# Kernel optimization log

Measured on AMD Instinct MI355X. Metric: run time of the kernel, lower is better.

Reference implementation:

```python
import jax, jax.numpy as jnp
import numpy as np

N_NODES = 20000
N_EDGES = 640000
D = 128


def setup_inputs() -> dict:
    key = jax.random.key(0)
    ks = jax.random.split(key, 8)
    scale = 1.0 / np.sqrt(D)
    x = jax.random.normal(ks[0], (N_NODES, D), dtype=jnp.float32)
    edge_index = jax.random.randint(ks[1], (2, N_EDGES), 0, N_NODES, dtype=jnp.int64)
    W1_rel = jax.random.normal(ks[2], (D, D), dtype=jnp.float32) * scale
    b1_rel = jnp.zeros((D,), dtype=jnp.float32)
    W1_root = jax.random.normal(ks[3], (D, D), dtype=jnp.float32) * scale
    W2_rel = jax.random.normal(ks[4], (D, D), dtype=jnp.float32) * scale
    b2_rel = jnp.zeros((D,), dtype=jnp.float32)
    W2_root = jax.random.normal(ks[5], (D, D), dtype=jnp.float32) * scale
    return {"x": x, "edge_index": edge_index,
            "W1_rel": W1_rel, "b1_rel": b1_rel, "W1_root": W1_root,
            "W2_rel": W2_rel, "b2_rel": b2_rel, "W2_root": W2_root}


def _graph_conv(x, src, dst, W_rel, b_rel, W_root):
    # sum-aggregate neighbor features: gather from src, scatter-add to dst
    agg = jax.ops.segment_sum(x[src], dst, num_segments=N_NODES)  # [N, D]
    # PyG GraphConv: lin_rel(agg) (with bias) + lin_root(x) (no bias)
    return agg @ W_rel + b_rel + x @ W_root


def reference(x, edge_index, W1_rel, b1_rel, W1_root, W2_rel, b2_rel, W2_root):
    src, dst = edge_index[0], edge_index[1]  # messages flow src (j) -> dst (i)
    h = jax.nn.relu(_graph_conv(x, src, dst, W1_rel, b1_rel, W1_root))
    out = _graph_conv(h, src, dst, W2_rel, b2_rel, W2_root)  # final ReLU stripped
    return out
```

## Files before the change

kernel.cpp:

```cpp
#include <hip/hip_runtime.h>

#define N_NODES 20000
#define N_EDGES 640000
#define D 128
#define CAP 128
#define NBINS 157
#define PA_BLOCKS 256
#define EPB 2500
#define SLABCAP 40

typedef __attribute__((ext_vector_type(8))) short bf16x8;
typedef __attribute__((ext_vector_type(4))) float f32x4;

__device__ __forceinline__ short f2bf(float f) {
    union { float f; unsigned u; } un; un.f = f;
    unsigned r = un.u + 0x7fff + ((un.u >> 16) & 1);
    return (short)(r >> 16);
}
__device__ __forceinline__ float bflo(unsigned u) { return __uint_as_float(u << 16); }
__device__ __forceinline__ float bfhi(unsigned u) { return __uint_as_float(u & 0xffff0000u); }

__global__ __launch_bounds__(256) void prep_kernel(
    const float* __restrict__ x,
    const int* __restrict__ src, const int* __restrict__ dst,
    const float* __restrict__ W1_rel, const float* __restrict__ W1_root,
    const float* __restrict__ W2_rel, const float* __restrict__ W2_root,
    unsigned* __restrict__ binned, int* __restrict__ cnts,
    short* __restrict__ xb, short* __restrict__ wpk1, short* __restrict__ wpk2)
{
    const int b = blockIdx.x;
    const int tid = threadIdx.x;
    if (b < PA_BLOCKS) {
        __shared__ int sOff[NBINS];
        for (int i = tid; i < NBINS; i += 256) sOff[i] = 0;
        __syncthreads();
        const int e0 = b * EPB;
        for (int idx = tid; idx < EPB; idx += 256) {
            int d = dst[e0 + idx];
            int s = src[e0 + idx];
            int bin = d >> 7;
            int off = atomicAdd(&sOff[bin], 1);
            if (off < SLABCAP)
                binned[(size_t)(bin * PA_BLOCKS + b) * SLABCAP + off] =
                    ((unsigned)(d & 127) << 16) | (unsigned)s;
        }
        __syncthreads();
        for (int i = tid; i < NBINS; i += 256) {
            int c = sOff[i];
            cnts[i * PA_BLOCKS + b] = (c > SLABCAP) ? SLABCAP : c;
        }
    } else if (b < PA_BLOCKS + 2500) {
        int i = (b - PA_BLOCKS) * 256 + tid;
        float4 v = ((const float4*)x)[i];
        ushort4 o;
        o.x = (unsigned short)f2bf(v.x);
        o.y = (unsigned short)f2bf(v.y);
        o.z = (unsigned short)f2bf(v.z);
        o.w = (unsigned short)f2bf(v.w);
        ((ushort4*)xb)[i] = o;
    } else {
        int pb  = b - (PA_BLOCKS + 2500);
        int job = pb >> 4;
        int idx = (pb & 15) * 256 + tid;
        const float* Wrel  = job ? W2_rel  : W1_rel;
        const float* Wroot = job ? W2_root : W1_root;
        short* Wpk = job ? wpk2 : wpk1;
        int lane = idx & 63;
        int ct   = (idx >> 6) & 7;
        int t    = idx >> 9;
        const float* W = (t < 4) ? Wrel : Wroot;
        int k0  = (t & 3) * 32 + (lane >> 4) * 8;
        int col = ct * 16 + (lane & 15);
        bf16x8 pk;
#pragma unroll
        for (int j = 0; j < 8; j++)
            pk[j] = f2bf(W[(size_t)(k0 + j) * D + col]);
        ((bf16x8*)Wpk)[idx] = pk;
    }
}

__global__ __launch_bounds__(256) void binplace_kernel(
    const unsigned* __restrict__ binned, const int* __restrict__ cnts,
    unsigned short* __restrict__ buckets, int* __restrict__ cnt)
{
    __shared__ int lcnt[128];
    const int bin = blockIdx.x;
    const int tid = threadIdx.x;
    if (tid < 128) lcnt[tid] = 0;
    __syncthreads();
    int c = cnts[bin * PA_BLOCKS + tid];
    const unsigned* rec = binned + (size_t)(bin * PA_BLOCKS + tid) * SLABCAP;
    for (int i = 0; i < c; i++) {
        unsigned u = rec[i];
        int nl = (int)(u >> 16);
        int slot = atomicAdd(&lcnt[nl], 1);
        if (slot < CAP)
            buckets[(((bin << 7) | nl) << 7) + slot] = (unsigned short)(u & 0xffffu);
    }
    __syncthreads();
    int node = (bin << 7) + tid;
    if (tid < 128 && node < N_NODES) {
        int n = lcnt[tid];
        cnt[node] = (n > CAP) ? CAP : n;
    }
}

template <bool RELU, bool OUT_BF16>
__global__ __launch_bounds__(512) void layer_kernel(
    const short* __restrict__ xin,
    const int* __restrict__ cnt,
    const unsigned short* __restrict__ buckets,
    const short* __restrict__ Wpk,
    const float* __restrict__ brel,
    void* __restrict__ outp)
{
    __shared__ short sAgg[16][136];

    const int tid = threadIdx.x;

    for (int half = 0; half < 2; half++) {
        const int bin  = blockIdx.x * 2 + half;
        const int row0 = bin * 16;
        if (half) __syncthreads();

        {
            const int hw   = tid >> 5;
            const int lane = tid & 31;
            const int node = row0 + hw;
            int n = cnt[node];
            n = (n > CAP) ? CAP : n;
            uint2 idxpk = *(const uint2*)(buckets + (node << 7) + lane * 4);

            float4 acc = make_float4(0.f, 0.f, 0.f, 0.f);
            int full8 = n & ~7;
            int i = 0;
            for (; i < full8; i += 8) {
                int baseLane = i >> 2;
                uint2 u[8];
#pragma unroll
                for (int q = 0; q < 8; q++) {
                    unsigned word = __shfl((q & 2) ? idxpk.y : idxpk.x,
                                           baseLane + (q >> 2), 32);
                    unsigned sidx = (q & 1) ? (word >> 16) : (word & 0xffffu);
                    u[q] = *(const uint2*)(xin + (size_t)sidx * D + lane * 4);
                }
#pragma unroll
                for (int q = 0; q < 8; q++) {
                    acc.x += bflo(u[q].x); acc.y += bfhi(u[q].x);
                    acc.z += bflo(u[q].y); acc.w += bfhi(u[q].y);
                }
            }
            if (i < n) {
                uint2 u[8];
#pragma unroll
                for (int q = 0; q < 8; q++) {
                    int j  = i + q;
                    int jc = (j < n) ? j : (n - 1);
                    unsigned word = __shfl((jc & 2) ? idxpk.y : idxpk.x,
                                           jc >> 2, 32);
                    unsigned sidx = (jc & 1) ? (word >> 16) : (word & 0xffffu);
                    u[q] = *(const uint2*)(xin + (size_t)sidx * D + lane * 4);
                }
#pragma unroll
                for (int q = 0; q < 8; q++) {
                    float m = (i + q < n) ? 1.f : 0.f;
                    acc.x += m * bflo(u[q].x); acc.y += m * bfhi(u[q].x);
                    acc.z += m * bflo(u[q].y); acc.w += m * bfhi(u[q].y);
                }
            }
            ushort4 o;
            o.x = (unsigned short)f2bf(acc.x);
            o.y = (unsigned short)f2bf(acc.y);
            o.z = (unsigned short)f2bf(acc.z);
            o.w = (unsigned short)f2bf(acc.w);
            *(ushort4*)&sAgg[hw][lane * 4] = o;
        }
        __syncthreads();

        const int wave = tid >> 6;
        const int lane = tid & 63;
        const int quad = lane >> 4;
        const int l16  = lane & 15;

        f32x4 acc = (f32x4){0.f, 0.f, 0.f, 0.f};
        const short* arow_x = xin + (size_t)(row0 + l16) * D + quad * 8;
        const bf16x8* wb = (const bf16x8*)Wpk + lane;

#pragma unroll
        for (int t = 0; t < 8; t++) {
            bf16x8 a;
            if (t < 4)
                a = *(const bf16x8*)&sAgg[l16][(t & 3) * 32 + quad * 8];
            else
                a = *(const bf16x8*)(arow_x + (t & 3) * 32);
            bf16x8 bfr = wb[(t * 8 + wave) * 64];
            acc = __builtin_amdgcn_mfma_f32_16x16x32_bf16(a, bfr, acc, 0, 0, 0);
        }

        const int col  = wave * 16 + l16;
        const int orow = row0 + quad * 4;
        const float bias = brel[col];
#pragma unroll
        for (int r = 0; r < 4; r++) {
            float v = acc[r] + bias;
            if (RELU) v = fmaxf(v, 0.f);
            if (OUT_BF16)
                ((short*)outp)[(size_t)(orow + r) * D + col] = f2bf(v);
            else
                ((float*)outp)[(size_t)(orow + r) * D + col] = v;
        }
    }
}

extern "C" void kernel_launch(void* const* d_in, const int* in_sizes, int n_in,
                              void* d_out, int out_size, void* d_ws, size_t ws_size,
                              hipStream_t stream) {
    const float* x       = (const float*)d_in[0];
    const int*   ei      = (const int*)  d_in[1];
    const float* W1_rel  = (const float*)d_in[2];
    const float* b1_rel  = (const float*)d_in[3];
    const float* W1_root = (const float*)d_in[4];
    const float* W2_rel  = (const float*)d_in[5];
    const float* b2_rel  = (const float*)d_in[6];
    const float* W2_root = (const float*)d_in[7];
    float* out = (float*)d_out;

    char* p = (char*)d_ws;
    short* xb   = (short*)p;  p += (size_t)N_NODES * D * 2;
    short* hb   = (short*)p;  p += (size_t)N_NODES * D * 2;
    short* wpk1 = (short*)p;  p += 65536;
    short* wpk2 = (short*)p;  p += 65536;
    int*   cnt  = (int*)p;    p += (size_t)N_NODES * 4;
    unsigned short* buckets = (unsigned short*)p;
    p += (size_t)NBINS * 128 * CAP * 2;
    unsigned* binned = (unsigned*)p;
    p += (size_t)NBINS * PA_BLOCKS * SLABCAP * 4;
    int* cnts = (int*)p;

    const int* src = ei;
    const int* dst = ei + N_EDGES;

    prep_kernel<<<PA_BLOCKS + 2500 + 32, 256, 0, stream>>>(
        x, src, dst, W1_rel, W1_root, W2_rel, W2_root,
        binned, cnts, xb, wpk1, wpk2);

    binplace_kernel<<<NBINS, 256, 0, stream>>>(binned, cnts, buckets, cnt);

    layer_kernel<true, true><<<625, 512, 0, stream>>>(
        xb, cnt, buckets, wpk1, b1_rel, (void*)hb);

    layer_kernel<false, false><<<625, 512, 0, stream>>>(
        hb, cnt, buckets, wpk2, b2_rel, (void*)out);
}
```

Before: 151.4 us.

## Fuse all stages into one persistent kernel with software grid barriers

Replaces the four separate launches (prep, binplace, two layer kernels) with a single persistent kernel of 512 blocks. Stages are separated by a spin-wait grid barrier on global atomics, reset each call by a memset. The edge binning is repartitioned to 512 blocks with smaller slabs, and the layer loop becomes grid-strided. This removes launch gaps and inter-kernel drain, but it depends on all blocks being co-resident, serialises the binplace stage onto 157 blocks while the rest wait, and the smaller slab capacity may drop edges for heavier bins.

```diff
diff --git a/kernel.cpp b/kernel.cpp
--- a/kernel.cpp
+++ b/kernel.cpp
@@ -5,9 +5,11 @@
 #define D 128
 #define CAP 128
 #define NBINS 157
-#define PA_BLOCKS 256
-#define EPB 2500
-#define SLABCAP 40
+#define NBLK 512
+#define NTHR 512
+#define EPB 1250
+#define SLABCAP 24
+#define LBINS (N_NODES / 16)
 
 typedef __attribute__((ext_vector_type(8))) short bf16x8;
 typedef __attribute__((ext_vector_type(4))) float f32x4;
@@ -20,108 +22,41 @@
 __device__ __forceinline__ float bflo(unsigned u) { return __uint_as_float(u << 16); }
 __device__ __forceinline__ float bfhi(unsigned u) { return __uint_as_float(u & 0xffff0000u); }
 
-__global__ __launch_bounds__(256) void prep_kernel(
-    const float* __restrict__ x,
-    const int* __restrict__ src, const int* __restrict__ dst,
-    const float* __restrict__ W1_rel, const float* __restrict__ W1_root,
-    const float* __restrict__ W2_rel, const float* __restrict__ W2_root,
-    unsigned* __restrict__ binned, int* __restrict__ cnts,
-    short* __restrict__ xb, short* __restrict__ wpk1, short* __restrict__ wpk2)
-{
-    const int b = blockIdx.x;
-    const int tid = threadIdx.x;
-    if (b < PA_BLOCKS) {
-        __shared__ int sOff[NBINS];
-        for (int i = tid; i < NBINS; i += 256) sOff[i] = 0;
-        __syncthreads();
-        const int e0 = b * EPB;
-        for (int idx = tid; idx < EPB; idx += 256) {
-            int d = dst[e0 + idx];
-            int s = src[e0 + idx];
-            int bin = d >> 7;
-            int off = atomicAdd(&sOff[bin], 1);
-            if (off < SLABCAP)
-                binned[(size_t)(bin * PA_BLOCKS + b) * SLABCAP + off] =
-                    ((unsigned)(d & 127) << 16) | (unsigned)s;
-        }
-        __syncthreads();
-        for (int i = tid; i < NBINS; i += 256) {
-            int c = sOff[i];
-            cnts[i * PA_BLOCKS + b] = (c > SLABCAP) ? SLABCAP : c;
-        }
-    } else if (b < PA_BLOCKS + 2500) {
-        int i = (b - PA_BLOCKS) * 256 + tid;
-        float4 v = ((const float4*)x)[i];
-        ushort4 o;
-        o.x = (unsigned short)f2bf(v.x);
-        o.y = (unsigned short)f2bf(v.y);
-        o.z = (unsigned short)f2bf(v.z);
-        o.w = (unsigned short)f2bf(v.w);
-        ((ushort4*)xb)[i] = o;
-    } else {
-        int pb  = b - (PA_BLOCKS + 2500);
-        int job = pb >> 4;
-        int idx = (pb & 15) * 256 + tid;
-        const float* Wrel  = job ? W2_rel  : W1_rel;
-        const float* Wroot = job ? W2_root : W1_root;
-        short* Wpk = job ? wpk2 : wpk1;
-        int lane = idx & 63;
-        int ct   = (idx >> 6) & 7;
-        int t    = idx >> 9;
-        const float* W = (t < 4) ? Wrel : Wroot;
-        int k0  = (t & 3) * 32 + (lane >> 4) * 8;
-        int col = ct * 16 + (lane & 15);
-        bf16x8 pk;
-#pragma unroll
-        for (int j = 0; j < 8; j++)
-            pk[j] = f2bf(W[(size_t)(k0 + j) * D + col]);
-        ((bf16x8*)Wpk)[idx] = pk;
-    }
-}
-
-__global__ __launch_bounds__(256) void binplace_kernel(
-    const unsigned* __restrict__ binned, const int* __restrict__ cnts,
-    unsigned short* __restrict__ buckets, int* __restrict__ cnt)
-{
-    __shared__ int lcnt[128];
-    const int bin = blockIdx.x;
-    const int tid = threadIdx.x;
-    if (tid < 128) lcnt[tid] = 0;
+union ShMem {
+    int   sOff[NBINS];
+    int   lcnt[128];
+    short sAgg[16][136];
+};
+
+__device__ __forceinline__ void grid_barrier(int* bar_cnt, int* bar_gen) {
     __syncthreads();
-    int c = cnts[bin * PA_BLOCKS + tid];
-    const unsigned* rec = binned + (size_t)(bin * PA_BLOCKS + tid) * SLABCAP;
-    for (int i = 0; i < c; i++) {
-        unsigned u = rec[i];
-        int nl = (int)(u >> 16);
-        int slot = atomicAdd(&lcnt[nl], 1);
-        if (slot < CAP)
-            buckets[(((bin << 7) | nl) << 7) + slot] = (unsigned short)(u & 0xffffu);
+    if (threadIdx.x == 0) {
+        __threadfence();
+        int g = atomicAdd(bar_gen, 0);
+        if (atomicAdd(bar_cnt, 1) == NBLK - 1) {
+            atomicExch(bar_cnt, 0);
+            atomicAdd(bar_gen, 1);
+        } else {
+            while (atomicAdd(bar_gen, 0) == g)
+                __builtin_amdgcn_s_sleep(8);
+        }
+        __threadfence();
     }
     __syncthreads();
-    int node = (bin << 7) + tid;
-    if (tid < 128 && node < N_NODES) {
-        int n = lcnt[tid];
-        cnt[node] = (n > CAP) ? CAP : n;
-    }
 }
 
 template <bool RELU, bool OUT_BF16>
-__global__ __launch_bounds__(512) void layer_kernel(
-    const short* __restrict__ xin,
-    const int* __restrict__ cnt,
+__device__ __forceinline__ void do_layer(
+    short (*sAgg)[136],
+    const short* __restrict__ xin, const int* __restrict__ cnt,
     const unsigned short* __restrict__ buckets,
-    const short* __restrict__ Wpk,
-    const float* __restrict__ brel,
+    const short* __restrict__ Wpk, const float* __restrict__ brel,
     void* __restrict__ outp)
 {
-    __shared__ short sAgg[16][136];
-
     const int tid = threadIdx.x;
-
-    for (int half = 0; half < 2; half++) {
-        const int bin  = blockIdx.x * 2 + half;
+    for (int bin = blockIdx.x; bin < LBINS; bin += NBLK) {
         const int row0 = bin * 16;
-        if (half) __syncthreads();
+        if (bin != (int)blockIdx.x) __syncthreads();
 
         {
             const int hw   = tid >> 5;
@@ -210,6 +145,106 @@
                 ((float*)outp)[(size_t)(orow + r) * D + col] = v;
         }
     }
+}
+
+__global__ __launch_bounds__(NTHR, 4) void mega_kernel(
+    const float* __restrict__ x,
+    const int* __restrict__ src, const int* __restrict__ dst,
+    const float* __restrict__ W1_rel, const float* __restrict__ W1_root,
+    const float* __restrict__ W2_rel, const float* __restrict__ W2_root,
+    const float* __restrict__ b1_rel, const float* __restrict__ b2_rel,
+    unsigned* __restrict__ binned, int* __restrict__ cnts,
+    unsigned short* __restrict__ buckets, int* __restrict__ cnt,
+    short* __restrict__ xb, short* __restrict__ hb,
+    short* __restrict__ wpk1, short* __restrict__ wpk2,
+    int* __restrict__ bar_cnt, int* __restrict__ bar_gen,
+    float* __restrict__ out)
+{
+    __shared__ ShMem sh;
+    const int b   = blockIdx.x;
+    const int tid = threadIdx.x;
+
+    {
+        for (int i = tid; i < NBINS; i += NTHR) sh.sOff[i] = 0;
+        __syncthreads();
+        const int e0 = b * EPB;
+        for (int idx = tid; idx < EPB; idx += NTHR) {
+            int d = dst[e0 + idx];
+            int s = src[e0 + idx];
+            int bin = d >> 7;
+            int off = atomicAdd(&sh.sOff[bin], 1);
+            if (off < SLABCAP)
+                binned[((size_t)b * NBINS + bin) * SLABCAP + off] =
+                    ((unsigned)(d & 127) << 16) | (unsigned)s;
+        }
+        __syncthreads();
+        for (int i = tid; i < NBINS; i += NTHR) {
+            int c = sh.sOff[i];
+            cnts[b * NBINS + i] = (c > SLABCAP) ? SLABCAP : c;
+        }
+    }
+    {
+        const int gtid = b * NTHR + tid;
+        for (int i = gtid; i < N_NODES * D / 4; i += NBLK * NTHR) {
+            float4 v = ((const float4*)x)[i];
+            ushort4 o;
+            o.x = (unsigned short)f2bf(v.x);
+            o.y = (unsigned short)f2bf(v.y);
+            o.z = (unsigned short)f2bf(v.z);
+            o.w = (unsigned short)f2bf(v.w);
+            ((ushort4*)xb)[i] = o;
+        }
+    }
+    {
+        const int gtid = b * NTHR + tid;
+        if (gtid < 8192) {
+            int job = gtid >> 12;
+            int idx = gtid & 4095;
+            const float* Wrel  = job ? W2_rel  : W1_rel;
+            const float* Wroot = job ? W2_root : W1_root;
+            short* Wpk = job ? wpk2 : wpk1;
+            int lane = idx & 63;
+            int ct   = (idx >> 6) & 7;
+            int t    = idx >> 9;
+            const float* W = (t < 4) ? Wrel : Wroot;
+            int k0  = (t & 3) * 32 + (lane >> 4) * 8;
+            int col = ct * 16 + (lane & 15);
+            bf16x8 pk;
+#pragma unroll
+            for (int j = 0; j < 8; j++)
+                pk[j] = f2bf(W[(size_t)(k0 + j) * D + col]);
+            ((bf16x8*)Wpk)[idx] = pk;
+        }
+    }
+    grid_barrier(bar_cnt, bar_gen);
+
+    if (b < NBINS) {
+        if (tid < 128) sh.lcnt[tid] = 0;
+        __syncthreads();
+        const int bin = b;
+        int c = cnts[tid * NBINS + bin];
+        const unsigned* rec = binned + ((size_t)tid * NBINS + bin) * SLABCAP;
+        for (int i = 0; i < c; i++) {
+            unsigned u = rec[i];
+            int nl = (int)(u >> 16);
+            int slot = atomicAdd(&sh.lcnt[nl], 1);
+            if (slot < CAP)
+                buckets[(((bin << 7) | nl) << 7) + slot] =
+                    (unsigned short)(u & 0xffffu);
+        }
+        __syncthreads();
+        int node = (bin << 7) + tid;
+        if (tid < 128 && node < N_NODES) {
+            int n = sh.lcnt[tid];
+            cnt[node] = (n > CAP) ? CAP : n;
+        }
+    }
+    grid_barrier(bar_cnt, bar_gen);
+
+    do_layer<true, true>(sh.sAgg, xb, cnt, buckets, wpk1, b1_rel, (void*)hb);
+    grid_barrier(bar_cnt, bar_gen);
+
+    do_layer<false, false>(sh.sAgg, hb, cnt, buckets, wpk2, b2_rel, (void*)out);
 }
 
 extern "C" void kernel_launch(void* const* d_in, const int* in_sizes, int n_in,
@@ -234,21 +269,18 @@
     unsigned short* buckets = (unsigned short*)p;
     p += (size_t)NBINS * 128 * CAP * 2;
     unsigned* binned = (unsigned*)p;
-    p += (size_t)NBINS * PA_BLOCKS * SLABCAP * 4;
-    int* cnts = (int*)p;
+    p += (size_t)NBLK * NBINS * SLABCAP * 4;
+    int* cnts = (int*)p;      p += (size_t)NBLK * NBINS * 4;
+    int* bar  = (int*)p;
+    int* bar_cnt = bar;
+    int* bar_gen = bar + 32;
 
     const int* src = ei;
     const int* dst = ei + N_EDGES;
 
-    prep_kernel<<<PA_BLOCKS + 2500 + 32, 256, 0, stream>>>(
-        x, src, dst, W1_rel, W1_root, W2_rel, W2_root,
-        binned, cnts, xb, wpk1, wpk2);
-
-    binplace_kernel<<<NBINS, 256, 0, stream>>>(binned, cnts, buckets, cnt);
-
-    layer_kernel<true, true><<<625, 512, 0, stream>>>(
-        xb, cnt, buckets, wpk1, b1_rel, (void*)hb);
-
-    layer_kernel<false, false><<<625, 512, 0, stream>>>(
-        hb, cnt, buckets, wpk2, b2_rel, (void*)out);
-}
+    hipMemsetAsync(bar, 0, 256, stream);
+    mega_kernel<<<NBLK, NTHR, 0, stream>>>(
+        x, src, dst, W1_rel, W1_root, W2_rel, W2_root, b1_rel, b2_rel,
+        binned, cnts, buckets, cnt, xb, hb, wpk1, wpk2,
+        bar_cnt, bar_gen, out);
+}
```

Result: slower. 205.1 us (+35.5%).

## Split neighbor lists by source half and gather halves in phased order

Applied to the files above, without the earlier changes.

The bin placement now stores sources below 10000 from the front of each node's bucket and sources at or above 10000 from the back, packing both counts into cnt. The layer kernel gathers the low-index sources first, hits a block barrier, then gathers the high-index sources, so all waves in a block touch a narrower slice of the feature table at a time for better cache locality. The layer kernel also drops its two-bins-per-block loop and launches twice as many blocks, one 16-row bin each. The extra barrier in the middle of the gather adds synchronisation and can stall waves whose nodes have uneven low/high counts.

```diff
diff --git a/kernel.cpp b/kernel.cpp
--- a/kernel.cpp
+++ b/kernel.cpp
@@ -8,6 +8,7 @@
 #define PA_BLOCKS 256
 #define EPB 2500
 #define SLABCAP 40
+#define SRC_SPLIT 10000
 
 typedef __attribute__((ext_vector_type(8))) short bf16x8;
 typedef __attribute__((ext_vector_type(4))) float f32x4;
@@ -83,25 +84,75 @@
     const unsigned* __restrict__ binned, const int* __restrict__ cnts,
     unsigned short* __restrict__ buckets, int* __restrict__ cnt)
 {
-    __shared__ int lcnt[128];
+    __shared__ int lo[128];
+    __shared__ int hi[128];
     const int bin = blockIdx.x;
     const int tid = threadIdx.x;
-    if (tid < 128) lcnt[tid] = 0;
+    if (tid < 128) { lo[tid] = 0; hi[tid] = 0; }
     __syncthreads();
     int c = cnts[bin * PA_BLOCKS + tid];
     const unsigned* rec = binned + (size_t)(bin * PA_BLOCKS + tid) * SLABCAP;
     for (int i = 0; i < c; i++) {
         unsigned u = rec[i];
         int nl = (int)(u >> 16);
-        int slot = atomicAdd(&lcnt[nl], 1);
-        if (slot < CAP)
-            buckets[(((bin << 7) | nl) << 7) + slot] = (unsigned short)(u & 0xffffu);
+        unsigned s = u & 0xffffu;
+        if ((int)s < SRC_SPLIT) {
+            int slot = atomicAdd(&lo[nl], 1);
+            if (slot < CAP)
+                buckets[(((bin << 7) | nl) << 7) + slot] = (unsigned short)s;
+        } else {
+            int slot = CAP - 1 - atomicAdd(&hi[nl], 1);
+            if (slot >= 0)
+                buckets[(((bin << 7) | nl) << 7) + slot] = (unsigned short)s;
+        }
     }
     __syncthreads();
     int node = (bin << 7) + tid;
     if (tid < 128 && node < N_NODES) {
-        int n = lcnt[tid];
-        cnt[node] = (n > CAP) ? CAP : n;
+        int nlo = lo[tid]; if (nlo > CAP) nlo = CAP;
+        int nhi = hi[tid]; if (nhi > CAP - nlo) nhi = CAP - nlo;
+        cnt[node] = nlo | (nhi << 16);
+    }
+}
+
+__device__ __forceinline__ void gather_range(
+    float4& acc, const short* __restrict__ xin,
+    uint2 idxpk, int lane, int start, int count)
+{
+    const int end = start + count;
+    int k = start;
+    const int full_end = start + (count & ~7);
+    for (; k < full_end; k += 8) {
+        uint2 u[8];
+#pragma unroll
+        for (int q = 0; q < 8; q++) {
+            int j = k + q;
+            unsigned word = __shfl((j & 2) ? idxpk.y : idxpk.x, j >> 2, 32);
+            unsigned sidx = (j & 1) ? (word >> 16) : (word & 0xffffu);
+            u[q] = *(const uint2*)(xin + (size_t)sidx * D + lane * 4);
+        }
+#pragma unroll
+        for (int q = 0; q < 8; q++) {
+            acc.x += bflo(u[q].x); acc.y += bfhi(u[q].x);
+            acc.z += bflo(u[q].y); acc.w += bfhi(u[q].y);
+        }
+    }
+    if (k < end) {
+        uint2 u[8];
+#pragma unroll
+        for (int q = 0; q < 8; q++) {
+            int j  = k + q;
+            int jc = (j < end) ? j : (end - 1);
+            unsigned word = __shfl((jc & 2) ? idxpk.y : idxpk.x, jc >> 2, 32);
+            unsigned sidx = (jc & 1) ? (word >> 16) : (word & 0xffffu);
+            u[q] = *(const uint2*)(xin + (size_t)sidx * D + lane * 4);
+        }
+#pragma unroll
+        for (int q = 0; q < 8; q++) {
+            float m = (k + q < end) ? 1.f : 0.f;
+            acc.x += m * bflo(u[q].x); acc.y += m * bfhi(u[q].x);
+            acc.z += m * bflo(u[q].y); acc.w += m * bfhi(u[q].y);
+        }
     }
 }
 
@@ -116,99 +167,63 @@
 {
     __shared__ short sAgg[16][136];
 
-    const int tid = threadIdx.x;
-
-    for (int half = 0; half < 2; half++) {
-        const int bin  = blockIdx.x * 2 + half;
-        const int row0 = bin * 16;
-        if (half) __syncthreads();
-
-        {
-            const int hw   = tid >> 5;
-            const int lane = tid & 31;
-            const int node = row0 + hw;
-            int n = cnt[node];
-            n = (n > CAP) ? CAP : n;
-            uint2 idxpk = *(const uint2*)(buckets + (node << 7) + lane * 4);
-
-            float4 acc = make_float4(0.f, 0.f, 0.f, 0.f);
-            int full8 = n & ~7;
-            int i = 0;
-            for (; i < full8; i += 8) {
-                int baseLane = i >> 2;
-                uint2 u[8];
-#pragma unroll
-                for (int q = 0; q < 8; q++) {
-                    unsigned word = __shfl((q & 2) ? idxpk.y : idxpk.x,
-                                           baseLane + (q >> 2), 32);
-                    unsigned sidx = (q & 1) ? (word >> 16) : (word & 0xffffu);
-                    u[q] = *(const uint2*)(xin + (size_t)sidx * D + lane * 4);
-                }
-#pragma unroll
-                for (int q = 0; q < 8; q++) {
-                    acc.x += bflo(u[q].x); acc.y += bfhi(u[q].x);
-                    acc.z += bflo(u[q].y); acc.w += bfhi(u[q].y);
-                }
-            }
-            if (i < n) {
-                uint2 u[8];
-#pragma unroll
-                for (int q = 0; q < 8; q++) {
-                    int j  = i + q;
-                    int jc = (j < n) ? j : (n - 1);
-                    unsigned word = __shfl((jc & 2) ? idxpk.y : idxpk.x,
-                                           jc >> 2, 32);
-                    unsigned sidx = (jc & 1) ? (word >> 16) : (word & 0xffffu);
-                    u[q] = *(const uint2*)(xin + (size_t)sidx * D + lane * 4);
-                }
-#pragma unroll
-                for (int q = 0; q < 8; q++) {
-                    float m = (i + q < n) ? 1.f : 0.f;
-                    acc.x += m * bflo(u[q].x); acc.y += m * bfhi(u[q].x);
-                    acc.z += m * bflo(u[q].y); acc.w += m * bfhi(u[q].y);
-                }
-            }
-            ushort4 o;
-            o.x = (unsigned short)f2bf(acc.x);
-            o.y = (unsigned short)f2bf(acc.y);
-            o.z = (unsigned short)f2bf(acc.z);
-            o.w = (unsigned short)f2bf(acc.w);
-            *(ushort4*)&sAgg[hw][lane * 4] = o;
-        }
+    const int tid  = threadIdx.x;
+    const int row0 = blockIdx.x * 16;
+
+    {
+        const int hw   = tid >> 5;
+        const int lane = tid & 31;
+        const int node = row0 + hw;
+        int nc  = cnt[node];
+        int nlo = nc & 0xffff;
+        int nhi = nc >> 16;
+        uint2 idxpk = *(const uint2*)(buckets + (node << 7) + lane * 4);
+
+        float4 acc = make_float4(0.f, 0.f, 0.f, 0.f);
+        gather_range(acc, xin, idxpk, lane, 0, nlo);
         __syncthreads();
-
-        const int wave = tid >> 6;
-        const int lane = tid & 63;
-        const int quad = lane >> 4;
-        const int l16  = lane & 15;
-
-        f32x4 acc = (f32x4){0.f, 0.f, 0.f, 0.f};
-        const short* arow_x = xin + (size_t)(row0 + l16) * D + quad * 8;
-        const bf16x8* wb = (const bf16x8*)Wpk + lane;
-
-#pragma unroll
-        for (int t = 0; t < 8; t++) {
-            bf16x8 a;
-            if (t < 4)
-                a = *(const bf16x8*)&sAgg[l16][(t & 3) * 32 + quad * 8];
-            else
-                a = *(const bf16x8*)(arow_x + (t & 3) * 32);
-            bf16x8 bfr = wb[(t * 8 + wave) * 64];
-            acc = __builtin_amdgcn_mfma_f32_16x16x32_bf16(a, bfr, acc, 0, 0, 0);
-        }
-
-        const int col  = wave * 16 + l16;
-        const int orow = row0 + quad * 4;
-        const float bias = brel[col];
-#pragma unroll
-        for (int r = 0; r < 4; r++) {
-            float v = acc[r] + bias;
-            if (RELU) v = fmaxf(v, 0.f);
-            if (OUT_BF16)
-                ((short*)outp)[(size_t)(orow + r) * D + col] = f2bf(v);
-            else
-                ((float*)outp)[(size_t)(orow + r) * D + col] = v;
-        }
+        gather_range(acc, xin, idxpk, lane, CAP - nhi, nhi);
+
+        ushort4 o;
+        o.x = (unsigned short)f2bf(acc.x);
+        o.y = (unsigned short)f2bf(acc.y);
+        o.z = (unsigned short)f2bf(acc.z);
+        o.w = (unsigned short)f2bf(acc.w);
+        *(ushort4*)&sAgg[hw][lane * 4] = o;
+    }
+    __syncthreads();
+
+    const int wave = tid >> 6;
+    const int lane = tid & 63;
+    const int quad = lane >> 4;
+    const int l16  = lane & 15;
+
+    f32x4 acc = (f32x4){0.f, 0.f, 0.f, 0.f};
+    const short* arow_x = xin + (size_t)(row0 + l16) * D + quad * 8;
+    const bf16x8* wb = (const bf16x8*)Wpk + lane;
+
+#pragma unroll
+    for (int t = 0; t < 8; t++) {
+        bf16x8 a;
+        if (t < 4)
+            a = *(const bf16x8*)&sAgg[l16][(t & 3) * 32 + quad * 8];
+        else
+            a = *(const bf16x8*)(arow_x + (t & 3) * 32);
+        bf16x8 bfr = wb[(t * 8 + wave) * 64];
+        acc = __builtin_amdgcn_mfma_f32_16x16x32_bf16(a, bfr, acc, 0, 0, 0);
+    }
+
+    const int col  = wave * 16 + l16;
+    const int orow = row0 + quad * 4;
+    const float bias = brel[col];
+#pragma unroll
+    for (int r = 0; r < 4; r++) {
+        float v = acc[r] + bias;
+        if (RELU) v = fmaxf(v, 0.f);
+        if (OUT_BF16)
+            ((short*)outp)[(size_t)(orow + r) * D + col] = f2bf(v);
+        else
+            ((float*)outp)[(size_t)(orow + r) * D + col] = v;
     }
 }
 
@@ -246,9 +261,9 @@
 
     binplace_kernel<<<NBINS, 256, 0, stream>>>(binned, cnts, buckets, cnt);
 
-    layer_kernel<true, true><<<625, 512, 0, stream>>>(
+    layer_kernel<true, true><<<1250, 512, 0, stream>>>(
         xb, cnt, buckets, wpk1, b1_rel, (void*)hb);
 
-    layer_kernel<false, false><<<625, 512, 0, stream>>>(
+    layer_kernel<false, false><<<1250, 512, 0, stream>>>(
         hb, cnt, buckets, wpk2, b2_rel, (void*)out);
 }
```

Measured after the change: 147.8 us, median of 2. 1.02x faster.
